# Performance work log

Hardware: AMD Instinct MI355X
Metric: run time of the kernel (lower is better)

Reference implementation:

```python
import jax, jax.numpy as jnp
import numpy as np
from jax import lax

K = 7          # kernel size
G = 12         # groups
EPS = 1e-5


def bn(x, gamma, beta, axes):
    # training-mode batch norm (torch default train() mode uses batch stats)
    mean = jnp.mean(x, axis=axes, keepdims=True)
    var = jnp.var(x, axis=axes, keepdims=True)
    shape = [1] * x.ndim
    shape[1 if x.ndim == 4 else -1] = -1
    g = gamma.reshape(shape)
    b = beta.reshape(shape)
    return g * (x - mean) * lax.rsqrt(var + EPS) + b


def setup_inputs() -> dict:
    key = jax.random.key(0)
    ks = jax.random.split(key, 12)
    B, C, H, Wd = 16, 192, 32, 32
    Cr = C // 4                      # reduce_mapping out channels = out_channels // reduce_ratio = 48
    flat = C * H * Wd                # 196608
    inp = {
        "x": jax.random.normal(ks[0], (B, C, H, Wd), jnp.float32),
        "Wr": jax.random.normal(ks[1], (Cr, C), jnp.float32) * 0.05,          # reduce_mapping 1x1 conv
        "gamma_s": jnp.ones((Cr,), jnp.float32),
        "beta_s": jnp.zeros((Cr,), jnp.float32),
        "Ws": jax.random.normal(ks[2], (K * K * G, Cr), jnp.float32) * 0.05,  # span_mapping 1x1 conv
        "W1": jax.random.normal(ks[3], (512, flat), jnp.float32) * 0.002,
        "b1": jnp.zeros((512,), jnp.float32),
        "g1": jnp.ones((512,), jnp.float32),
        "beta1": jnp.zeros((512,), jnp.float32),
        "W2": jax.random.normal(ks[4], (128, 512), jnp.float32) * 0.04,
        "b2": jnp.zeros((128,), jnp.float32),
        "g2": jnp.ones((128,), jnp.float32),
        "beta2": jnp.zeros((128,), jnp.float32),
        "W3": jax.random.normal(ks[5], (17, 128), jnp.float32) * 0.09,
        "b3": jnp.zeros((17,), jnp.float32),
    }
    return inp


def reference(x, Wr, gamma_s, beta_s, Ws, W1, b1, g1, beta1, W2, b2, g2, beta2, W3, b3):
    B, C, H, Wd = x.shape
    Cg = C // G
    # unfold (im2col) with kernel 7, pad 3, stride 1, dil 1 -> [B, C*K*K, H, W]
    # channel ordering (c, kh, kw) matches torch.nn.Unfold
    patches = lax.conv_general_dilated_patches(x, (K, K), (1, 1), [(K // 2, K // 2)] * 2)
    unf = patches.reshape(B, G, Cg, K * K, H, Wd)
    # kernel generation path: 1x1 reduce conv -> BN+ReLU -> 1x1 span conv
    red = jnp.einsum('bchw,oc->bohw', x, Wr)
    red = jax.nn.relu(bn(red, gamma_s, beta_s, (0, 2, 3)))
    ker = jnp.einsum('bchw,oc->bohw', red, Ws).reshape(B, G, K * K, H, Wd)
    # involution: per-pixel kernel multiply + sum over K*K
    out = jnp.einsum('bgkhw,bgckhw->bgchw', ker, unf).reshape(B, C, H, Wd)
    # classifier head
    flat = out.reshape(B, -1)
    h = jax.nn.relu(bn(flat @ W1.T + b1, g1, beta1, (0,)))
    h = jax.nn.relu(bn(h @ W2.T + b2, g2, beta2, (0,)))
    return h @ W3.T + b3
```

## Files before the change

### kernel.cpp

```cpp
#include <hip/hip_runtime.h>

#define EPS 1e-5f

typedef float v4f __attribute__((ext_vector_type(4)));

__global__ __launch_bounds__(256) void k_reduce_conv(
    const float* __restrict__ x, const float* __restrict__ Wr,
    float* __restrict__ red, float* __restrict__ spart)
{
  int ob = blockIdx.x >> 6;
  int pb = blockIdx.x & 63;
  int o0 = ob * 6;
  int pix = (pb << 8) + threadIdx.x;
  int b = pix >> 10;
  int hw = pix & 1023;
  const float* xp = x + ((size_t)b * 192) * 1024 + hw;
  float acc[6] = {0.f, 0.f, 0.f, 0.f, 0.f, 0.f};
  for (int c = 0; c < 192; ++c) {
    float xv = xp[(size_t)c * 1024];
#pragma unroll
    for (int j = 0; j < 6; ++j)
      acc[j] = fmaf(xv, Wr[(o0 + j) * 192 + c], acc[j]);
  }
#pragma unroll
  for (int j = 0; j < 6; ++j)
    red[(size_t)(o0 + j) * 16384 + pix] = acc[j];

  int t = threadIdx.x, lane = t & 63, wid = t >> 6;
  float sv[6], qv[6];
#pragma unroll
  for (int j = 0; j < 6; ++j) { sv[j] = acc[j]; qv[j] = acc[j] * acc[j]; }
#pragma unroll
  for (int off = 32; off > 0; off >>= 1)
#pragma unroll
    for (int j = 0; j < 6; ++j) {
      sv[j] += __shfl_down(sv[j], off);
      qv[j] += __shfl_down(qv[j], off);
    }
  __shared__ float ps[4][12];
  if (lane == 0)
#pragma unroll
    for (int j = 0; j < 6; ++j) { ps[wid][j] = sv[j]; ps[wid][6 + j] = qv[j]; }
  __syncthreads();
  if (t < 12) {
    float v = ps[0][t] + ps[1][t] + ps[2][t] + ps[3][t];
    int j = t % 6, s = t / 6;
    spart[(size_t)(s * 48 + o0 + j) * 64 + pb] = v;
  }
}

__global__ __launch_bounds__(256) void k_invol(
    const float* __restrict__ x, const float* __restrict__ red,
    const float* __restrict__ spart, const float* __restrict__ gamma_s,
    const float* __restrict__ beta_s, const float* __restrict__ Ws,
    float* __restrict__ flat)
{
  __shared__ __align__(16) float xt[196 * 20];
  __shared__ __align__(16) float redn[64 * 52];
  __shared__ __align__(16) float kt[49 * 64];
  __shared__ float sstats[96];

  int bx = blockIdx.x;
  int tile = bx & 15;
  int g = (bx >> 4) % 12;
  int b = bx / 192;
  int th = (tile >> 2) * 8, tw = (tile & 3) * 8;
  int t = threadIdx.x;

  if (t < 96) {
    const v4f* p = (const v4f*)(spart + (size_t)t * 64);
    v4f s4 = p[0];
#pragma unroll
    for (int i = 1; i < 16; ++i) s4 += p[i];
    sstats[t] = s4.x + s4.y + s4.z + s4.w;
  }

  for (int idx = t; idx < 16 * 196; idx += 256) {
    int c = idx / 196, s = idx - c * 196;
    int r = s / 14, q = s - r * 14;
    int sh = th + r - 3, sw = tw + q - 3;
    float v = 0.f;
    if (sh >= 0 && sh < 32 && sw >= 0 && sw < 32)
      v = x[(((size_t)b * 192 + g * 16 + c) << 10) + (sh << 5) + sw];
    xt[s * 20 + c] = v;
  }
  __syncthreads();

  for (int idx = t; idx < 64 * 48; idx += 256) {
    int p = idx & 63, o = idx >> 6;
    int py = p >> 3, px = p & 7;
    float mean = sstats[o] * (1.f / 16384.f);
    float var = fmaf(-mean, mean, sstats[48 + o] * (1.f / 16384.f));
    float sc = gamma_s[o] * rsqrtf(var + EPS);
    float sh_ = fmaf(-mean, sc, beta_s[o]);
    float v = red[(size_t)o * 16384 + (b << 10) + ((th + py) << 5) + (tw + px)];
    redn[p * 52 + o] = fmaxf(fmaf(v, sc, sh_), 0.f);
  }
  __syncthreads();

  {
    int p = t & 63;
    int kg = __builtin_amdgcn_readfirstlane(t >> 6);
    int k0 = kg * 13;
    float acc[13];
#pragma unroll
    for (int j = 0; j < 13; ++j) acc[j] = 0.f;
    const float* wsp = Ws + (size_t)(g * 49 + k0) * 48;
    for (int o4 = 0; o4 < 48; o4 += 4) {
      v4f rv = *(const v4f*)&redn[p * 52 + o4];
#pragma unroll
      for (int j = 0; j < 13; ++j)
        if (k0 + j < 49) {
          acc[j] = fmaf(rv.x, wsp[j * 48 + o4 + 0], acc[j]);
          acc[j] = fmaf(rv.y, wsp[j * 48 + o4 + 1], acc[j]);
          acc[j] = fmaf(rv.z, wsp[j * 48 + o4 + 2], acc[j]);
          acc[j] = fmaf(rv.w, wsp[j * 48 + o4 + 3], acc[j]);
        }
    }
#pragma unroll
    for (int j = 0; j < 13; ++j)
      if (k0 + j < 49) kt[(k0 + j) * 64 + p] = acc[j];
  }
  __syncthreads();

  {
    int p = t & 63, cq = t >> 6;
    int c0 = cq * 4;
    int py = p >> 3, px = p & 7;
    float a0 = 0.f, a1 = 0.f, a2 = 0.f, a3 = 0.f;
#pragma unroll
    for (int k = 0; k < 49; ++k) {
      int dh = k / 7, dw = k - dh * 7;
      float kv = kt[k * 64 + p];
      const v4f xv = *(const v4f*)&xt[((py + dh) * 14 + px + dw) * 20 + c0];
      a0 = fmaf(kv, xv.x, a0);
      a1 = fmaf(kv, xv.y, a1);
      a2 = fmaf(kv, xv.z, a2);
      a3 = fmaf(kv, xv.w, a3);
    }
    size_t base = (((size_t)b * 192 + g * 16 + c0) << 10) + ((th + py) << 5) + (tw + px);
    flat[base] = a0;
    flat[base + 1024] = a1;
    flat[base + 2048] = a2;
    flat[base + 3072] = a3;
  }
}

__global__ __launch_bounds__(256, 2) void k_gemm1(
    const float* __restrict__ flat, const float* __restrict__ W1,
    float* __restrict__ h1part)
{
  int kc = blockIdx.x;
  int n0 = blockIdx.y * 4;
  int t = threadIdx.x;
  int kt = t & 127;
  int bg = t >> 7;
  int b0 = bg * 8;

  const v4f* W1v = (const v4f*)W1;
  const v4f* flatv = (const v4f*)flat;

  float acc[4][8];
#pragma unroll
  for (int n = 0; n < 4; ++n)
#pragma unroll
    for (int j = 0; j < 8; ++j) acc[n][j] = 0.f;

  int kv = kc * 6144 + kt;

  v4f w[4], wn[4], f[8];
#pragma unroll
  for (int n = 0; n < 4; ++n)
    w[n] = W1v[(size_t)(n0 + n) * 49152 + kv];

#define GEMM1_PHASE(CUR, NXT, PRE)                                         \
  {                                                                        \
    _Pragma("unroll")                                                      \
    for (int j = 0; j < 8; ++j)                                            \
      f[j] = flatv[(size_t)(b0 + j) * 49152 + kv];                         \
    if (PRE) {                                                             \
      _Pragma("unroll")                                                    \
      for (int n = 0; n < 4; ++n)                                          \
        NXT[n] = W1v[(size_t)(n0 + n) * 49152 + kv + 128];                 \
    }                                                                      \
    _Pragma("unroll")                                                      \
    for (int j = 0; j < 8; ++j)                                            \
      _Pragma("unroll")                                                    \
      for (int n = 0; n < 4; ++n) {                                        \
        acc[n][j] = fmaf(CUR[n].x, f[j].x, acc[n][j]);                     \
        acc[n][j] = fmaf(CUR[n].y, f[j].y, acc[n][j]);                     \
        acc[n][j] = fmaf(CUR[n].z, f[j].z, acc[n][j]);                     \
        acc[n][j] = fmaf(CUR[n].w, f[j].w, acc[n][j]);                     \
      }                                                                    \
    kv += 128;                                                             \
  }

#pragma unroll 1
  for (int it = 0; it < 24; ++it) {
    GEMM1_PHASE(w, wn, true)
    GEMM1_PHASE(wn, w, (it < 23))
  }
#undef GEMM1_PHASE

  __shared__ float rbuf[256 * 33];
#pragma unroll
  for (int nn = 0; nn < 4; ++nn)
#pragma unroll
    for (int j = 0; j < 8; ++j)
      rbuf[t * 33 + nn * 8 + j] = acc[nn][j];
  __syncthreads();
  {
    int v = t >> 2;
    int c = v & 31, bgsel = v >> 5;
    int i = t & 3;
    float s = 0.f;
#pragma unroll
    for (int r = 0; r < 32; ++r)
      s += rbuf[(bgsel * 128 + i + (r << 2)) * 33 + c];
    s += __shfl_down(s, 2, 4);
    s += __shfl_down(s, 1, 4);
    if (i == 0) {
      int nn = c >> 3, j = c & 7;
      int b = bgsel * 8 + j;
      h1part[(size_t)kc * 8192 + b * 512 + n0 + nn] = s;
    }
  }
}

__global__ __launch_bounds__(256) void k_gemm2(
    const float* __restrict__ h1part, const float* __restrict__ g1,
    const float* __restrict__ beta1, const float* __restrict__ W2,
    float* __restrict__ h2pre)
{
  __shared__ __align__(16) float h1s[2][512];
  int t = threadIdx.x;
  int b0 = blockIdx.x * 2;

#pragma unroll
  for (int rep = 0; rep < 2; ++rep) {
    int n = rep * 256 + t;
    float v[16];
#pragma unroll
    for (int b = 0; b < 16; ++b) v[b] = 0.f;
    for (int y = 0; y < 8; ++y)
#pragma unroll
      for (int b = 0; b < 16; ++b)
        v[b] += h1part[(size_t)y * 8192 + b * 512 + n];
    float s = 0.f;
#pragma unroll
    for (int b = 0; b < 16; ++b) s += v[b];
    float mean = s * (1.f / 16.f);
    float q = 0.f;
#pragma unroll
    for (int b = 0; b < 16; ++b) { float d = v[b] - mean; q = fmaf(d, d, q); }
    float inv = rsqrtf(q * (1.f / 16.f) + EPS);
    float sc = g1[n] * inv, sh = beta1[n];
    h1s[0][n] = fmaxf(fmaf(v[b0] - mean, sc, sh), 0.f);
    h1s[1][n] = fmaxf(fmaf(v[b0 + 1] - mean, sc, sh), 0.f);
  }
  __syncthreads();

  int m = t & 127, bsel = t >> 7;
  const v4f* W2v = (const v4f*)W2;
  v4f sa = {0.f, 0.f, 0.f, 0.f};
  for (int nv = 0; nv < 128; ++nv) {
    v4f wv = W2v[(size_t)m * 128 + nv];
    v4f hv = *(const v4f*)&h1s[bsel][nv * 4];
    sa.x = fmaf(hv.x, wv.x, sa.x);
    sa.y = fmaf(hv.y, wv.y, sa.y);
    sa.z = fmaf(hv.z, wv.z, sa.z);
    sa.w = fmaf(hv.w, wv.w, sa.w);
  }
  h2pre[(b0 + bsel) * 128 + m] = (sa.x + sa.y) + (sa.z + sa.w);
}

__global__ __launch_bounds__(320) void k_tail(
    const float* __restrict__ h2pre, const float* __restrict__ g2,
    const float* __restrict__ beta2, const float* __restrict__ W3,
    const float* __restrict__ b3, float* __restrict__ out)
{
  __shared__ float h2[16 * 128];
  int t = threadIdx.x;
  if (t < 128) {
    float v[16];
    float s = 0.f;
#pragma unroll
    for (int b = 0; b < 16; ++b) { v[b] = h2pre[b * 128 + t]; s += v[b]; }
    float mean = s * (1.f / 16.f);
    float q = 0.f;
#pragma unroll
    for (int b = 0; b < 16; ++b) { float d = v[b] - mean; q = fmaf(d, d, q); }
    float inv = rsqrtf(q * (1.f / 16.f) + EPS);
    float sc = g2[t] * inv, sh = beta2[t];
#pragma unroll
    for (int b = 0; b < 16; ++b)
      h2[b * 128 + t] = fmaxf(fmaf(v[b] - mean, sc, sh), 0.f);
  }
  __syncthreads();
  if (t < 272) {
    int b = t / 17, j = t - b * 17;
    float s = b3[j];
    const float* hp = h2 + b * 128;
    const float* wp = W3 + j * 128;
#pragma unroll 4
    for (int m = 0; m < 128; ++m) s = fmaf(hp[m], wp[m], s);
    out[t] = s;
  }
}

extern "C" void kernel_launch(void* const* d_in, const int* in_sizes, int n_in,
                              void* d_out, int out_size, void* d_ws, size_t ws_size,
                              hipStream_t stream)
{
  const float* x       = (const float*)d_in[0];
  const float* Wr      = (const float*)d_in[1];
  const float* gamma_s = (const float*)d_in[2];
  const float* beta_s  = (const float*)d_in[3];
  const float* Ws      = (const float*)d_in[4];
  const float* W1      = (const float*)d_in[5];
  const float* g1      = (const float*)d_in[7];
  const float* beta1   = (const float*)d_in[8];
  const float* W2      = (const float*)d_in[9];
  const float* g2      = (const float*)d_in[11];
  const float* beta2   = (const float*)d_in[12];
  const float* W3      = (const float*)d_in[13];
  const float* b3      = (const float*)d_in[14];

  float* ws = (float*)d_ws;
  float* red    = ws;
  float* flat   = red + 786432;
  float* spart  = flat + 3145728;
  float* h1part = spart + 6144;
  float* h2pre  = h1part + 65536;

  k_reduce_conv<<<512, 256, 0, stream>>>(x, Wr, red, spart);
  k_invol<<<3072, 256, 0, stream>>>(x, red, spart, gamma_s, beta_s, Ws, flat);
  k_gemm1<<<dim3(8, 128), 256, 0, stream>>>(flat, W1, h1part);
  k_gemm2<<<8, 256, 0, stream>>>(h1part, g1, beta1, W2, h2pre);
  k_tail<<<1, 320, 0, stream>>>(h2pre, g2, beta2, W3, b3, (float*)d_out);
}
```

Baseline: 327.5 us.

## Retile gemm1 so each thread covers all 16 batches, with deeper W1 prefetch

Each block of the large flat×W1 GEMM now covers 8 output neurons instead of 4. Each thread computes all 16 batch rows for 4 neurons, so every flat load is reused across twice as many outputs and the grid is halved. W1 loads become non-temporal and are prefetched two stages ahead with a three-buffer rotation, and sched_barriers pin the load order. The shared-memory reduction is redone per neuron in four passes. The change raises register pressure and drops the two-blocks-per-CU launch bound, which may reduce occupancy.

```diff
diff --git a/kernel.cpp b/kernel.cpp
--- a/kernel.cpp
+++ b/kernel.cpp
@@ -146,45 +146,51 @@
   }
 }
 
-__global__ __launch_bounds__(256, 2) void k_gemm1(
+__global__ __launch_bounds__(256) void k_gemm1(
     const float* __restrict__ flat, const float* __restrict__ W1,
     float* __restrict__ h1part)
 {
   int kc = blockIdx.x;
-  int n0 = blockIdx.y * 4;
+  int n0 = blockIdx.y * 8;
   int t = threadIdx.x;
   int kt = t & 127;
   int bg = t >> 7;
-  int b0 = bg * 8;
+  int nb = n0 + bg * 4;
 
   const v4f* W1v = (const v4f*)W1;
   const v4f* flatv = (const v4f*)flat;
 
-  float acc[4][8];
+  float acc[4][16];
 #pragma unroll
   for (int n = 0; n < 4; ++n)
 #pragma unroll
-    for (int j = 0; j < 8; ++j) acc[n][j] = 0.f;
+    for (int j = 0; j < 16; ++j) acc[n][j] = 0.f;
 
   int kv = kc * 6144 + kt;
 
-  v4f w[4], wn[4], f[8];
+  v4f wA[4], wB[4], wC[4], f[16];
 #pragma unroll
   for (int n = 0; n < 4; ++n)
-    w[n] = W1v[(size_t)(n0 + n) * 49152 + kv];
-
-#define GEMM1_PHASE(CUR, NXT, PRE)                                         \
+    wA[n] = __builtin_nontemporal_load(&W1v[(size_t)(nb + n) * 49152 + kv]);
+#pragma unroll
+  for (int n = 0; n < 4; ++n)
+    wB[n] = __builtin_nontemporal_load(&W1v[(size_t)(nb + n) * 49152 + kv + 128]);
+
+#define GEMM1_PHASE(CUR, DST, PRE)                                         \
   {                                                                        \
     _Pragma("unroll")                                                      \
-    for (int j = 0; j < 8; ++j)                                            \
-      f[j] = flatv[(size_t)(b0 + j) * 49152 + kv];                         \
+    for (int j = 0; j < 16; ++j)                                           \
+      f[j] = flatv[(size_t)j * 49152 + kv];                                \
+    __builtin_amdgcn_sched_barrier(0);                                     \
     if (PRE) {                                                             \
       _Pragma("unroll")                                                    \
       for (int n = 0; n < 4; ++n)                                          \
-        NXT[n] = W1v[(size_t)(n0 + n) * 49152 + kv + 128];                 \
+        DST[n] = __builtin_nontemporal_load(                               \
+            &W1v[(size_t)(nb + n) * 49152 + kv + 256]);                    \
     }                                                                      \
+    __builtin_amdgcn_sched_barrier(0);                                     \
     _Pragma("unroll")                                                      \
-    for (int j = 0; j < 8; ++j)                                            \
+    for (int j = 0; j < 16; ++j)                                           \
       _Pragma("unroll")                                                    \
       for (int n = 0; n < 4; ++n) {                                        \
         acc[n][j] = fmaf(CUR[n].x, f[j].x, acc[n][j]);                     \
@@ -196,34 +202,33 @@
   }
 
 #pragma unroll 1
-  for (int it = 0; it < 24; ++it) {
-    GEMM1_PHASE(w, wn, true)
-    GEMM1_PHASE(wn, w, (it < 23))
+  for (int it = 0; it < 16; ++it) {
+    GEMM1_PHASE(wA, wC, true)
+    GEMM1_PHASE(wB, wA, (it < 15))
+    GEMM1_PHASE(wC, wB, (it < 15))
   }
 #undef GEMM1_PHASE
 
-  __shared__ float rbuf[256 * 33];
-#pragma unroll
-  for (int nn = 0; nn < 4; ++nn)
-#pragma unroll
-    for (int j = 0; j < 8; ++j)
-      rbuf[t * 33 + nn * 8 + j] = acc[nn][j];
-  __syncthreads();
-  {
-    int v = t >> 2;
-    int c = v & 31, bgsel = v >> 5;
-    int i = t & 3;
+  __shared__ float rbuf[256 * 17];
+#pragma unroll 1
+  for (int nn = 0; nn < 4; ++nn) {
+    __syncthreads();
+#pragma unroll
+    for (int j = 0; j < 16; ++j)
+      rbuf[t * 17 + j] = acc[nn][j];
+    __syncthreads();
+    int o = t >> 3;
+    int i = t & 7;
+    int bsel = o >> 4, b = o & 15;
     float s = 0.f;
 #pragma unroll
-    for (int r = 0; r < 32; ++r)
-      s += rbuf[(bgsel * 128 + i + (r << 2)) * 33 + c];
-    s += __shfl_down(s, 2, 4);
-    s += __shfl_down(s, 1, 4);
-    if (i == 0) {
-      int nn = c >> 3, j = c & 7;
-      int b = bgsel * 8 + j;
-      h1part[(size_t)kc * 8192 + b * 512 + n0 + nn] = s;
-    }
+    for (int r = 0; r < 16; ++r)
+      s += rbuf[(bsel * 128 + i + (r << 3)) * 17 + b];
+    s += __shfl_down(s, 4, 8);
+    s += __shfl_down(s, 2, 8);
+    s += __shfl_down(s, 1, 8);
+    if (i == 0)
+      h1part[(size_t)kc * 8192 + b * 512 + n0 + bsel * 4 + nn] = s;
   }
 }
 
@@ -335,7 +340,7 @@
 
   k_reduce_conv<<<512, 256, 0, stream>>>(x, Wr, red, spart);
   k_invol<<<3072, 256, 0, stream>>>(x, red, spart, gamma_s, beta_s, Ws, flat);
-  k_gemm1<<<dim3(8, 128), 256, 0, stream>>>(flat, W1, h1part);
+  k_gemm1<<<dim3(8, 64), 256, 0, stream>>>(flat, W1, h1part);
   k_gemm2<<<8, 256, 0, stream>>>(h1part, g1, beta1, W2, h2pre);
   k_tail<<<1, 320, 0, stream>>>(h2pre, g2, beta2, W3, b3, (float*)d_out);
 }
```

Measured after the change: 317.9 us. 1.03x faster.
